# Performance work log

Measured on AMD Instinct MI355X. Metric: run time of the kernel, lower is better.

## Reference

```python
import jax, jax.numpy as jnp
import numpy as np

B, S, E, H = 2, 2048, 1024, 16
HD = E // H            # 64
LAMBDA_INIT = 0.8
EPS = 1e-6


def setup_inputs() -> dict:
    key = jax.random.key(0)
    ks = jax.random.split(key, 8)
    return {
        "x": jax.random.normal(ks[0], (B, S, E), dtype=jnp.float32),
        "w_qkv": jax.random.normal(ks[1], (E, 3 * E), dtype=jnp.float32) * (E ** -0.5),
        "wo": jax.random.normal(ks[2], (E, E), dtype=jnp.float32) * (E ** -0.5),
        "lambda_q1": jax.random.normal(ks[3], (HD,), dtype=jnp.float32) * 0.1,
        "lambda_q2": jax.random.normal(ks[4], (HD,), dtype=jnp.float32) * 0.1,
        "lambda_k1": jax.random.normal(ks[5], (HD,), dtype=jnp.float32) * 0.1,
        "lambda_k2": jax.random.normal(ks[6], (HD,), dtype=jnp.float32) * 0.1,
        "norm_w": jnp.ones((H, HD), dtype=jnp.float32),
    }


def reference(x, w_qkv, wo, lambda_q1, lambda_q2, lambda_k1, lambda_k2, norm_w):
    b, s, e = x.shape
    qkv = x @ w_qkv                                   # [b, s, 3e]
    q, k, v = jnp.split(qkv, 3, axis=-1)
    def to_heads(t):
        return t.reshape(b, s, H, HD).transpose(0, 2, 1, 3)  # [b, H, s, hd]
    q, k, v = to_heads(q), to_heads(k), to_heads(v)
    q1, q2 = jnp.split(q, 2, axis=-1)                 # [b, H, s, hd/2]
    k1, k2 = jnp.split(k, 2, axis=-1)
    scale = 1.0 / jnp.sqrt(jnp.asarray(HD, dtype=x.dtype))  # note: full head_dim, as in source
    a1 = jax.nn.softmax(jnp.einsum('bhsd,bhtd->bhst', q1, k1) * scale, axis=-1)
    a2 = jax.nn.softmax(jnp.einsum('bhsd,bhtd->bhst', q2, k2) * scale, axis=-1)
    lam = jnp.exp(jnp.dot(lambda_q1, lambda_k1)) - jnp.exp(jnp.dot(lambda_q2, lambda_k2)) + LAMBDA_INIT
    a = a1 - lam * a2                                 # [b, H, s, s]
    out = jnp.einsum('bhst,bhtd->bhsd', a, v)         # [b, H, s, hd]
    # per-head RMSNorm, scaled by (1 - lambda_init)
    rms = jnp.sqrt(jnp.mean(out * out, axis=-1, keepdims=True) + EPS)
    out_n = (out / rms) * norm_w[None, :, None, :] * (1.0 - LAMBDA_INIT)
    # replicate source's cat(dim=1) -> transpose(1,2) -> view(b, s, e)
    out_cat = out_n.reshape(b, H * s, HD)             # concat of per-head [b, s, hd]
    out_final = out_cat.transpose(0, 2, 1).reshape(b, s, e)
    return out_final @ wo
```

## Files before the change

kernel.cpp:

```cpp
#include <hip/hip_runtime.h>
#include <math.h>

#define B_ 2
#define S_ 2048
#define E_ 1024
#define H_ 16
#define HD_ 64
#define LAMBDA_INIT 0.8f
#define EPS_ 1e-6f

typedef __attribute__((ext_vector_type(8))) short short8;
typedef __attribute__((ext_vector_type(4))) float floatx4;
typedef __attribute__((ext_vector_type(16))) float floatx16;

__device__ __forceinline__ unsigned short f2bf(float f) {
  unsigned u = __float_as_uint(f);
  u += 0x7FFFu + ((u >> 16) & 1u);
  return (unsigned short)(u >> 16);
}

__device__ __forceinline__ void gl_lds16(const void* g, void* l) {
  __builtin_amdgcn_global_load_lds((const __attribute__((address_space(1))) void*)g,
                                   (__attribute__((address_space(3))) void*)l,
                                   16, 0, 0);
}

__global__ __launch_bounds__(256) void cast_bf16(const float* __restrict__ in,
                                                 unsigned short* __restrict__ out,
                                                 int n4) {
  for (int i = blockIdx.x * 256 + threadIdx.x; i < n4; i += gridDim.x * 256) {
    float4 v = ((const float4*)in)[i];
    ushort4 w;
    w.x = f2bf(v.x); w.y = f2bf(v.y); w.z = f2bf(v.z); w.w = f2bf(v.w);
    ((ushort4*)out)[i] = w;
  }
}

__global__ __launch_bounds__(256) void transpose_cast(const float* __restrict__ in,
                                                      unsigned short* __restrict__ out,
                                                      int R, int C) {
  __shared__ float tile[64][65];
  const int tid = threadIdx.x;
  const int c0 = blockIdx.x * 64;
  const int r0 = blockIdx.y * 64;
#pragma unroll
  for (int it = 0; it < 16; it++) {
    int e = tid + it * 256;
    int rr = e >> 6, cc = e & 63;
    tile[rr][cc] = in[(size_t)(r0 + rr) * C + c0 + cc];
  }
  __syncthreads();
#pragma unroll
  for (int it = 0; it < 16; it++) {
    int e = tid + it * 256;
    int rr = e >> 6, cc = e & 63;
    out[(size_t)(c0 + rr) * R + r0 + cc] = f2bf(tile[cc][rr]);
  }
}

template <bool BF16OUT, int BNT>
__global__ __launch_bounds__(256, BNT == 64 ? 2 : 1) void gemm_bt(
    const unsigned short* __restrict__ A, const unsigned short* __restrict__ Bt,
    void* __restrict__ C, int M, int N, int K) {
  __shared__ __align__(16) unsigned short As[128 * 64];
  __shared__ __align__(16) unsigned short Bs[BNT * 64];
  const int tid = threadIdx.x;
  const int wave = tid >> 6, lane = tid & 63;
  const int lane15 = lane & 15, quad = lane >> 4;
  const int m0 = blockIdx.y * 128;
  const int n0 = blockIdx.x * BNT;
  const int wm = (wave & 1) * 64, wn = (wave >> 1) * (BNT / 2);
  const int NI = BNT / 32;

  floatx4 acc[4][NI];
#pragma unroll
  for (int mi = 0; mi < 4; mi++)
#pragma unroll
    for (int ni = 0; ni < NI; ni++) acc[mi][ni] = (floatx4)0.0f;

  const int rsA = wave * 32 + (lane >> 3);
  const int rsB = wave * (BNT / 4) + (lane >> 3);
  const int cph = lane & 7;

  for (int k0 = 0; k0 < K; k0 += 64) {
    __syncthreads();
#pragma unroll
    for (int j = 0; j < 4; j++) {
      int r = rsA + j * 8;
      int cl = cph ^ (r & 7);
      gl_lds16(A + (size_t)(m0 + r) * K + k0 + cl * 8, &As[(wave * 32 + j * 8) * 64]);
    }
#pragma unroll
    for (int j = 0; j < BNT / 32; j++) {
      int r = rsB + j * 8;
      int cl = cph ^ (r & 7);
      gl_lds16(Bt + (size_t)(n0 + r) * K + k0 + cl * 8,
               &Bs[(wave * (BNT / 4) + j * 8) * 64]);
    }
    __syncthreads();

#pragma unroll
    for (int ks = 0; ks < 2; ks++) {
      short8 af[4], bf[NI];
#pragma unroll
      for (int mi = 0; mi < 4; mi++) {
        int r = wm + mi * 16 + lane15;
        int phys = (ks * 4 + quad) ^ (r & 7);
        af[mi] = *(const short8*)(&As[r * 64 + phys * 8]);
      }
#pragma unroll
      for (int ni = 0; ni < NI; ni++) {
        int r = wn + ni * 16 + lane15;
        int phys = (ks * 4 + quad) ^ (r & 7);
        bf[ni] = *(const short8*)(&Bs[r * 64 + phys * 8]);
      }
#pragma unroll
      for (int mi = 0; mi < 4; mi++)
#pragma unroll
        for (int ni = 0; ni < NI; ni++)
          acc[mi][ni] = __builtin_amdgcn_mfma_f32_16x16x32_bf16(af[mi], bf[ni],
                                                                acc[mi][ni], 0, 0, 0);
    }
  }

#pragma unroll
  for (int mi = 0; mi < 4; mi++)
#pragma unroll
    for (int ni = 0; ni < NI; ni++)
#pragma unroll
      for (int reg = 0; reg < 4; reg++) {
        int row = m0 + wm + mi * 16 + quad * 4 + reg;
        int col = n0 + wn + ni * 16 + lane15;
        float v = acc[mi][ni][reg];
        if (BF16OUT)
          ((unsigned short*)C)[(size_t)row * N + col] = f2bf(v);
        else
          ((float*)C)[(size_t)row * N + col] = v;
      }
}

__global__ __launch_bounds__(512, 4) void flash_attn_mfma(
    const unsigned short* __restrict__ qkB, const unsigned short* __restrict__ vTB,
    const float* __restrict__ lq1, const float* __restrict__ lq2,
    const float* __restrict__ lk1, const float* __restrict__ lk2,
    const float* __restrict__ norm_w, float* __restrict__ out_n) {
  __shared__ __align__(16) unsigned short KV[2][2][64 * 64];
  __shared__ float Lex[4][64];

  const int tid = threadIdx.x;
  const int wave = tid >> 6, lane = tid & 63;
  const int l31 = lane & 31, hi = lane >> 5;
  const int qsub = wave >> 1, sw = wave & 1;

  const int bid = (blockIdx.x & 7) * 64 + (blockIdx.x >> 3);
  const int qt = bid & 15;
  const int h = (bid >> 4) & 15;
  const int b = bid >> 8;
  const int q0 = qt * 128;

  float a1 = 0.f, a2 = 0.f;
  for (int d = 0; d < HD_; d++) {
    a1 += lq1[d] * lk1[d];
    a2 += lq2[d] * lk2[d];
  }
  const float lam = __expf(a1) - __expf(a2) + LAMBDA_INIT;

  short8 qf[2];
  {
    const unsigned short* qrow =
        qkB + (size_t)(b * S_ + q0 + qsub * 32 + l31) * 2048 + h * 64 + sw * 32;
#pragma unroll
    for (int cs = 0; cs < 2; cs++)
      qf[cs] = *(const short8*)(qrow + cs * 16 + hi * 8);
  }

  floatx16 accO[2];
#pragma unroll
  for (int n = 0; n < 2; n++) accO[n] = (floatx16)0.0f;
  float lsum = 0.f;
  const floatx16 zero16 = (floatx16)0.0f;

  const int srow = tid >> 3;
  const int scol = tid & 7;
  const size_t kgbase = (size_t)(b * S_) * 2048 + 1024 + h * 64;
  const size_t vgbase = (size_t)h * 64 * 4096 + b * 2048;

#define STAGE(t_, buf_)                                                        \
  {                                                                            \
    const size_t kg_ = kgbase + (size_t)(t_) * 64 * 2048;                      \
    const size_t vg_ = vgbase + (size_t)(t_) * 64;                             \
    const int cl_ = scol ^ (srow & 7);                                         \
    gl_lds16(qkB + kg_ + (size_t)srow * 2048 + cl_ * 8,                        \
             &KV[buf_][0][(wave * 8) * 64]);                                   \
    gl_lds16(vTB + vg_ + (size_t)srow * 4096 + cl_ * 8,                        \
             &KV[buf_][1][(wave * 8) * 64]);                                   \
  }

  STAGE(0, 0);
  __syncthreads();

  int cur = 0;
  for (int t = 0; t < S_ / 64; t++) {
    if (t < S_ / 64 - 1) STAGE(t + 1, cur ^ 1);
    const unsigned short* Kc = &KV[cur][0][0];
    const unsigned short* Vc = &KV[cur][1][0];

#pragma unroll
    for (int kb = 0; kb < 2; kb++) {
      const int krow = kb * 32 + l31;
      const int kx = krow & 7;
      floatx16 accS = zero16;
#pragma unroll
      for (int cs = 0; cs < 2; cs++) {
        const int pc = (sw * 4 + cs * 2 + hi) ^ kx;
        const short8 kf = *(const short8*)(Kc + krow * 64 + pc * 8);
        accS = __builtin_amdgcn_mfma_f32_32x32x16_bf16(kf, qf[cs], accS, 0, 0, 0);
      }
      unsigned w[8];
      float ls = 0.f;
#pragma unroll
      for (int i = 0; i < 8; i++) {
        float p0 = __expf(accS[2 * i] * 0.125f);
        float p1 = __expf(accS[2 * i + 1] * 0.125f);
        ls += p0 + p1;
        asm("v_cvt_pk_bf16_f32 %0, %1, %2" : "=v"(w[i]) : "v"(p0), "v"(p1));
      }
      lsum += ls;
      asm volatile("v_permlane32_swap_b32 %0, %1" : "+v"(w[0]), "+v"(w[2]));
      asm volatile("v_permlane32_swap_b32 %0, %1" : "+v"(w[1]), "+v"(w[3]));
      asm volatile("v_permlane32_swap_b32 %0, %1" : "+v"(w[4]), "+v"(w[6]));
      asm volatile("v_permlane32_swap_b32 %0, %1" : "+v"(w[5]), "+v"(w[7]));
      uint4 u0 = make_uint4(w[0], w[1], w[2], w[3]);
      uint4 u1 = make_uint4(w[4], w[5], w[6], w[7]);
      short8 pf0 = __builtin_bit_cast(short8, u0);
      short8 pf1 = __builtin_bit_cast(short8, u1);
#pragma unroll
      for (int ks2 = 0; ks2 < 2; ks2++) {
        const short8 pa = ks2 ? pf1 : pf0;
#pragma unroll
        for (int n = 0; n < 2; n++) {
          const int vrow = n * 32 + l31;
          const int pc = (kb * 4 + ks2 * 2 + hi) ^ (vrow & 7);
          const short8 vf = *(const short8*)(Vc + vrow * 64 + pc * 8);
          accO[n] = __builtin_amdgcn_mfma_f32_32x32x16_bf16(pa, vf, accO[n], 0, 0, 0);
        }
      }
    }
    __syncthreads();
    cur ^= 1;
  }
#undef STAGE

  lsum += __shfl_xor(lsum, 32, 64);

  float* LF = (float*)&KV[0][0][0];
  if (sw == 1) {
    Lex[qsub][lane] = lsum;
#pragma unroll
    for (int n = 0; n < 2; n++)
#pragma unroll
      for (int r = 0; r < 16; r++)
        LF[qsub * 2048 + (n * 16 + r) * 64 + lane] = accO[n][r];
  }
  __syncthreads();

  if (sw == 0) {
    const float ls2v = Lex[qsub][lane];
    const float* nw = norm_w + h * HD_;
    const float nw0 = nw[l31], nw1 = nw[32 + l31];
#pragma unroll
    for (int r = 0; r < 16; r++) {
      const int qr = (r & 3) + 8 * (r >> 2) + 4 * hi;
      const float s1 = __shfl(lsum, qr, 64);
      const float s2 = __shfl(ls2v, qr, 64);
      const float inv1 = 1.0f / s1;
      const float c2 = lam / s2;
      const float b0 = LF[qsub * 2048 + (0 * 16 + r) * 64 + lane];
      const float b1 = LF[qsub * 2048 + (1 * 16 + r) * 64 + lane];
      float o0 = accO[0][r] * inv1 - b0 * c2;
      float o1 = accO[1][r] * inv1 - b1 * c2;
      float ss = o0 * o0 + o1 * o1;
#pragma unroll
      for (int msk = 1; msk <= 16; msk <<= 1) ss += __shfl_xor(ss, msk, 64);
      const float rsc = (1.0f - LAMBDA_INIT) * rsqrtf(ss * (1.0f / 64.0f) + EPS_);
      float* dst = out_n + ((size_t)(b * H_ + h) * S_ + q0 + qsub * 32 + qr) * HD_;
      dst[l31] = o0 * rsc * nw0;
      dst[32 + l31] = o1 * rsc * nw1;
    }
  }
}

__global__ __launch_bounds__(256) void reshape_out(const float* __restrict__ out_n,
                                                   unsigned short* __restrict__ hidden) {
  __shared__ float tile[64][65];
  const int tid = threadIdx.x;
  const int bi = blockIdx.x;
  const int tb = bi & 31;
  const int h = (bi >> 5) & 15;
  const int b = bi >> 9;
  const int t0 = tb * 64;
  const float* src = out_n + (((size_t)b * H_ + h) * S_ + t0) * HD_;
#pragma unroll
  for (int rr = 0; rr < 16; rr++) {
    int e = tid + rr * 256;
    tile[e >> 6][e & 63] = src[e];
  }
  __syncthreads();
  unsigned short* dst = hidden + (size_t)b * (S_ * E_) + h * S_ + t0;
#pragma unroll
  for (int rr = 0; rr < 16; rr++) {
    int e = tid + rr * 256;
    int d = e >> 6, tt = e & 63;
    dst[(size_t)d * (H_ * S_) + tt] = f2bf(tile[tt][d]);
  }
}

extern "C" void kernel_launch(void* const* d_in, const int* in_sizes, int n_in,
                              void* d_out, int out_size, void* d_ws, size_t ws_size,
                              hipStream_t stream) {
  const float* x = (const float*)d_in[0];
  const float* w_qkv = (const float*)d_in[1];
  const float* wo = (const float*)d_in[2];
  const float* lq1 = (const float*)d_in[3];
  const float* lq2 = (const float*)d_in[4];
  const float* lk1 = (const float*)d_in[5];
  const float* lk2 = (const float*)d_in[6];
  const float* norm_w = (const float*)d_in[7];
  float* out = (float*)d_out;

  unsigned short* xB = (unsigned short*)d_ws;
  unsigned short* WT = xB + (size_t)4096 * 1024;
  unsigned short* woT = WT + (size_t)3072 * 1024;
  unsigned short* qkB = woT + (size_t)1024 * 1024;
  unsigned short* vTB = qkB + (size_t)4096 * 2048;
  unsigned short* hidB = vTB + (size_t)1024 * 4096;
  float* out_n = (float*)(hidB + (size_t)4096 * 1024);

  cast_bf16<<<1024, 256, 0, stream>>>(x, xB, 4096 * 1024 / 4);
  transpose_cast<<<dim3(48, 16), 256, 0, stream>>>(w_qkv, WT, 1024, 3072);
  transpose_cast<<<dim3(16, 16), 256, 0, stream>>>(wo, woT, 1024, 1024);

  gemm_bt<true, 128><<<dim3(2048 / 128, 4096 / 128), 256, 0, stream>>>(
      xB, WT, (void*)qkB, 4096, 2048, 1024);
  gemm_bt<true, 64><<<dim3(4096 / 64, 1024 / 128), 256, 0, stream>>>(
      WT + (size_t)2048 * 1024, xB, (void*)vTB, 1024, 4096, 1024);

  flash_attn_mfma<<<B_ * H_ * (S_ / 128), 512, 0, stream>>>(qkB, vTB, lq1, lq2, lk1,
                                                            lk2, norm_w, out_n);
  reshape_out<<<B_ * H_ * (S_ / 64), 256, 0, stream>>>(out_n, hidB);
  gemm_bt<false, 64><<<dim3(1024 / 64, 4096 / 128), 256, 0, stream>>>(
      hidB, woT, (void*)out, 4096, 1024, 1024);
}
```

Measured before the change: 236.4 us.

## Fuse output reshape into attention epilogue and merge prep kernels

The attention kernel now stages the normalized head output in shared memory and writes the transposed bf16 hidden layout directly. This removes the fp32 intermediate buffer and the separate reshape kernel. The three casting and transpose prep kernels are merged into one launch that dispatches on block index. The change cuts global memory round trips and launch overhead, but adds about 33 KB of shared memory per attention block, which may lower occupancy.

```diff
diff --git a/kernel.cpp b/kernel.cpp
--- a/kernel.cpp
+++ b/kernel.cpp
@@ -10,6 +10,7 @@
 #define EPS_ 1e-6f
 
 typedef __attribute__((ext_vector_type(8))) short short8;
+typedef __attribute__((ext_vector_type(8))) unsigned short ushort8v;
 typedef __attribute__((ext_vector_type(4))) float floatx4;
 typedef __attribute__((ext_vector_type(16))) float floatx16;
 
@@ -25,24 +26,37 @@
                                    16, 0, 0);
 }
 
-__global__ __launch_bounds__(256) void cast_bf16(const float* __restrict__ in,
-                                                 unsigned short* __restrict__ out,
-                                                 int n4) {
-  for (int i = blockIdx.x * 256 + threadIdx.x; i < n4; i += gridDim.x * 256) {
-    float4 v = ((const float4*)in)[i];
-    ushort4 w;
-    w.x = f2bf(v.x); w.y = f2bf(v.y); w.z = f2bf(v.z); w.w = f2bf(v.w);
-    ((ushort4*)out)[i] = w;
-  }
-}
-
-__global__ __launch_bounds__(256) void transpose_cast(const float* __restrict__ in,
-                                                      unsigned short* __restrict__ out,
-                                                      int R, int C) {
+__global__ __launch_bounds__(256) void prep(const float* __restrict__ x,
+                                            const float* __restrict__ w_qkv,
+                                            const float* __restrict__ wo,
+                                            unsigned short* __restrict__ xB,
+                                            unsigned short* __restrict__ WT,
+                                            unsigned short* __restrict__ woT) {
   __shared__ float tile[64][65];
   const int tid = threadIdx.x;
-  const int c0 = blockIdx.x * 64;
-  const int r0 = blockIdx.y * 64;
+  const int bid = blockIdx.x;
+  if (bid < 1024) {
+    const int n4 = 4096 * 1024 / 4;
+    for (int i = bid * 256 + tid; i < n4; i += 1024 * 256) {
+      float4 v = ((const float4*)x)[i];
+      ushort4 w;
+      w.x = f2bf(v.x); w.y = f2bf(v.y); w.z = f2bf(v.z); w.w = f2bf(v.w);
+      ((ushort4*)xB)[i] = w;
+    }
+    return;
+  }
+  const float* in;
+  unsigned short* out;
+  int R, C, bx, by;
+  if (bid < 1792) {
+    in = w_qkv; out = WT; R = 1024; C = 3072;
+    int t = bid - 1024; bx = t % 48; by = t / 48;
+  } else {
+    in = wo; out = woT; R = 1024; C = 1024;
+    int t = bid - 1792; bx = t % 16; by = t / 16;
+  }
+  const int c0 = bx * 64;
+  const int r0 = by * 64;
 #pragma unroll
   for (int it = 0; it < 16; it++) {
     int e = tid + it * 256;
@@ -143,9 +157,10 @@
     const unsigned short* __restrict__ qkB, const unsigned short* __restrict__ vTB,
     const float* __restrict__ lq1, const float* __restrict__ lq2,
     const float* __restrict__ lk1, const float* __restrict__ lk2,
-    const float* __restrict__ norm_w, float* __restrict__ out_n) {
+    const float* __restrict__ norm_w, unsigned short* __restrict__ hid) {
   __shared__ __align__(16) unsigned short KV[2][2][64 * 64];
   __shared__ float Lex[4][64];
+  __shared__ float LF2[64][130];
 
   const int tid = threadIdx.x;
   const int wave = tid >> 6, lane = tid & 63;
@@ -283,35 +298,24 @@
 #pragma unroll
       for (int msk = 1; msk <= 16; msk <<= 1) ss += __shfl_xor(ss, msk, 64);
       const float rsc = (1.0f - LAMBDA_INIT) * rsqrtf(ss * (1.0f / 64.0f) + EPS_);
-      float* dst = out_n + ((size_t)(b * H_ + h) * S_ + q0 + qsub * 32 + qr) * HD_;
-      dst[l31] = o0 * rsc * nw0;
-      dst[32 + l31] = o1 * rsc * nw1;
-    }
-  }
-}
-
-__global__ __launch_bounds__(256) void reshape_out(const float* __restrict__ out_n,
-                                                   unsigned short* __restrict__ hidden) {
-  __shared__ float tile[64][65];
-  const int tid = threadIdx.x;
-  const int bi = blockIdx.x;
-  const int tb = bi & 31;
-  const int h = (bi >> 5) & 15;
-  const int b = bi >> 9;
-  const int t0 = tb * 64;
-  const float* src = out_n + (((size_t)b * H_ + h) * S_ + t0) * HD_;
-#pragma unroll
-  for (int rr = 0; rr < 16; rr++) {
-    int e = tid + rr * 256;
-    tile[e >> 6][e & 63] = src[e];
+      LF2[l31][qsub * 32 + qr] = o0 * rsc * nw0;
+      LF2[32 + l31][qsub * 32 + qr] = o1 * rsc * nw1;
+    }
   }
   __syncthreads();
-  unsigned short* dst = hidden + (size_t)b * (S_ * E_) + h * S_ + t0;
-#pragma unroll
-  for (int rr = 0; rr < 16; rr++) {
-    int e = tid + rr * 256;
-    int d = e >> 6, tt = e & 63;
-    dst[(size_t)d * (H_ * S_) + tt] = f2bf(tile[tt][d]);
+
+  {
+    const int d = tid >> 3, g = tid & 7;
+    unsigned short* dst =
+        hid + (size_t)b * (S_ * E_) + (size_t)d * (H_ * S_) + h * S_ + q0 + g * 16;
+    ushort8v v0, v1;
+#pragma unroll
+    for (int j = 0; j < 8; j++) {
+      v0[j] = f2bf(LF2[d][g * 16 + j]);
+      v1[j] = f2bf(LF2[d][g * 16 + 8 + j]);
+    }
+    *(ushort8v*)(dst) = v0;
+    *(ushort8v*)(dst + 8) = v1;
   }
 }
 
@@ -334,11 +338,8 @@
   unsigned short* qkB = woT + (size_t)1024 * 1024;
   unsigned short* vTB = qkB + (size_t)4096 * 2048;
   unsigned short* hidB = vTB + (size_t)1024 * 4096;
-  float* out_n = (float*)(hidB + (size_t)4096 * 1024);
-
-  cast_bf16<<<1024, 256, 0, stream>>>(x, xB, 4096 * 1024 / 4);
-  transpose_cast<<<dim3(48, 16), 256, 0, stream>>>(w_qkv, WT, 1024, 3072);
-  transpose_cast<<<dim3(16, 16), 256, 0, stream>>>(wo, woT, 1024, 1024);
+
+  prep<<<2048, 256, 0, stream>>>(x, w_qkv, wo, xB, WT, woT);
 
   gemm_bt<true, 128><<<dim3(2048 / 128, 4096 / 128), 256, 0, stream>>>(
       xB, WT, (void*)qkB, 4096, 2048, 1024);
@@ -346,8 +347,7 @@
       WT + (size_t)2048 * 1024, xB, (void*)vTB, 1024, 4096, 1024);
 
   flash_attn_mfma<<<B_ * H_ * (S_ / 128), 512, 0, stream>>>(qkB, vTB, lq1, lq2, lk1,
-                                                            lk2, norm_w, out_n);
-  reshape_out<<<B_ * H_ * (S_ / 64), 256, 0, stream>>>(out_n, hidB);
+                                                            lk2, norm_w, hidB);
   gemm_bt<false, 64><<<dim3(1024 / 64, 4096 / 128), 256, 0, stream>>>(
       hidB, woT, (void*)out, 4096, 1024, 1024);
 }
```

Result: faster. 227.8 us (-3.6%).
